# Optimization experiments

Hardware: AMD Instinct MI355X
Metric: run time of the kernel (lower is better)

## Reference

```python
import jax, jax.numpy as jnp
import numpy as np

D = 1024      # hidden_size
H = 16        # num_attention_heads
HD = D // H   # head_dim
FF = 4096     # intermediate_size
EPS = 1e-5

def layernorm(x, g, b):
    mu = jnp.mean(x, axis=-1, keepdims=True)
    var = jnp.mean(jnp.square(x - mu), axis=-1, keepdims=True)
    return (x - mu) * jax.lax.rsqrt(var + EPS) * g + b

def setup_inputs() -> dict:
    key = jax.random.key(0)
    ks = jax.random.split(key, 16)
    s = 0.02
    return {
        "x":   jax.random.normal(ks[0], (4, 1024, D), jnp.float32),
        "wq":  jax.random.normal(ks[1], (D, D), jnp.float32) * s,
        "bq":  jnp.zeros((D,), jnp.float32),
        "wk":  jax.random.normal(ks[2], (D, D), jnp.float32) * s,
        "bk":  jnp.zeros((D,), jnp.float32),
        "wv":  jax.random.normal(ks[3], (D, D), jnp.float32) * s,
        "bv":  jnp.zeros((D,), jnp.float32),
        "wo":  jax.random.normal(ks[4], (D, D), jnp.float32) * s,
        "bo":  jnp.zeros((D,), jnp.float32),
        "w1":  jax.random.normal(ks[5], (D, FF), jnp.float32) * s,
        "b1":  jnp.zeros((FF,), jnp.float32),
        "w2":  jax.random.normal(ks[6], (FF, D), jnp.float32) * s,
        "b2":  jnp.zeros((D,), jnp.float32),
        "ln1_g": jnp.ones((D,), jnp.float32),
        "ln1_b": jnp.zeros((D,), jnp.float32),
        "ln2_g": jnp.ones((D,), jnp.float32),
        "ln2_b": jnp.zeros((D,), jnp.float32),
    }

def reference(x, wq, bq, wk, bk, wv, bv, wo, bo, w1, b1, w2, b2,
              ln1_g, ln1_b, ln2_g, ln2_b):
    B, S, _ = x.shape
    # --- pre-LN multi-head attention (per-head linears fused as one GEMM) ---
    h = layernorm(x, ln1_g, ln1_b)
    q = (h @ wq + bq).reshape(B, S, H, HD).transpose(0, 2, 1, 3)  # [B,H,S,hd]
    k = (h @ wk + bk).reshape(B, S, H, HD).transpose(0, 2, 1, 3)
    v = (h @ wv + bv).reshape(B, S, H, HD).transpose(0, 2, 1, 3)
    scores = jnp.einsum('bhqd,bhkd->bhqk', q, k) / np.sqrt(HD).astype(x.dtype)
    weights = jax.nn.softmax(scores, axis=-1)  # dropout p=0 -> identity
    attn = jnp.einsum('bhqk,bhkd->bhqd', weights, v)
    attn = attn.transpose(0, 2, 1, 3).reshape(B, S, D)
    x = x + attn @ wo + bo
    # --- pre-LN feed-forward with exact GELU ---
    h2 = layernorm(x, ln2_g, ln2_b)
    ffn = jax.nn.gelu(h2 @ w1 + b1, approximate=False) @ w2 + b2
    return x + ffn
```

## Files before the change

### kernel.cpp

```cpp
#include <hip/hip_runtime.h>
#include <hip/hip_bf16.h>
#include <cstdint>

#define S_LEN  1024
#define DMODEL 1024
#define NTOK   4096
#define NHEAD  16
#define HDIM   64
#define FFDIM  4096
#define NBATCH 4
#define QSCALE 0.1803368801f

using bf16x8 = __attribute__((ext_vector_type(8))) short;
using f32x4  = __attribute__((ext_vector_type(4))) float;

__device__ __forceinline__ ushort f2bf(float f) {
  union { float f; uint32_t u; } a; a.f = f;
  uint32_t u = a.u;
  u += 0x7FFFu + ((u >> 16) & 1u);
  return (ushort)(u >> 16);
}
__device__ __forceinline__ ushort f2bf_hw(float f) {
  uint32_t r;
  asm("v_cvt_pk_bf16_f32 %0, %1, %1" : "=v"(r) : "v"(f));
  return (ushort)r;
}
__device__ __forceinline__ float bf2f(ushort u) {
  union { uint32_t u; float f; } c; c.u = ((uint32_t)u) << 16; return c.f;
}
__device__ __forceinline__ void st_out(float* C, long i, float v) { C[i] = v; }
__device__ __forceinline__ void st_out(ushort* C, long i, float v) { C[i] = f2bf(v); }

__device__ __forceinline__ void gld_lds16(const void* g, void* l) {
  __builtin_amdgcn_global_load_lds((const __attribute__((address_space(1))) void*)g,
                                   (__attribute__((address_space(3))) void*)l, 16, 0, 0);
}

__global__ __launch_bounds__(256) void ln_kernel(const float* __restrict__ x,
    const float* __restrict__ g, const float* __restrict__ b,
    ushort* __restrict__ out) {
  int row = blockIdx.x;
  int tid = threadIdx.x;
  const float4* xr = (const float4*)(x + (long)row * DMODEL);
  float4 v = xr[tid];
  float s  = v.x + v.y + v.z + v.w;
  float s2 = v.x*v.x + v.y*v.y + v.z*v.z + v.w*v.w;
  for (int off = 32; off; off >>= 1) { s += __shfl_down(s, off); s2 += __shfl_down(s2, off); }
  __shared__ float red[8];
  int wid = tid >> 6, lane = tid & 63;
  if (lane == 0) { red[wid] = s; red[wid + 4] = s2; }
  __syncthreads();
  if (tid == 0) {
    red[0] = red[0] + red[1] + red[2] + red[3];
    red[4] = red[4] + red[5] + red[6] + red[7];
  }
  __syncthreads();
  float mu  = red[0] * (1.0f / DMODEL);
  float var = red[4] * (1.0f / DMODEL) - mu * mu;
  float rs  = rsqrtf(var + 1e-5f);
  float4 gg = ((const float4*)g)[tid];
  float4 bb = ((const float4*)b)[tid];
  ushort4 o;
  o.x = f2bf((v.x - mu) * rs * gg.x + bb.x);
  o.y = f2bf((v.y - mu) * rs * gg.y + bb.y);
  o.z = f2bf((v.z - mu) * rs * gg.z + bb.z);
  o.w = f2bf((v.w - mu) * rs * gg.w + bb.w);
  ((ushort4*)(out + (long)row * DMODEL))[tid] = o;
}

__global__ __launch_bounds__(256) void concat3(const float* __restrict__ a,
    const float* __restrict__ b, const float* __restrict__ c, float* __restrict__ o) {
  int i = blockIdx.x * 256 + threadIdx.x;
  o[i] = (i < 1024) ? a[i] : ((i < 2048) ? b[i - 1024] : c[i - 2048]);
}

template <int NP>
__global__ __launch_bounds__(256) void reduce_add(
    const ushort* __restrict__ parts, const float* __restrict__ bias,
    float* __restrict__ out) {
  long i = (long)blockIdx.x * 256 + threadIdx.x;
  const long PSTRIDE = (long)NTOK * DMODEL / 4;
  float4 acc = ((const float4*)out)[i];
  float4 b = ((const float4*)bias)[i & 255];
  acc.x += b.x; acc.y += b.y; acc.z += b.z; acc.w += b.w;
#pragma unroll
  for (int z = 0; z < NP; ++z) {
    ushort4 u = ((const ushort4*)parts)[z * PSTRIDE + i];
    acc.x += bf2f(u.x); acc.y += bf2f(u.y); acc.z += bf2f(u.z); acc.w += bf2f(u.w);
  }
  ((float4*)out)[i] = acc;
}

template <int NP>
__global__ __launch_bounds__(256) void reduce_ln(
    const ushort* __restrict__ parts, const float* __restrict__ xres,
    const float* __restrict__ bias, float* __restrict__ out,
    const float* __restrict__ g, const float* __restrict__ bln,
    ushort* __restrict__ hout) {
  int row = blockIdx.x, tid = threadIdx.x;
  long i = (long)row * 256 + tid;
  const long PSTRIDE = (long)NTOK * DMODEL / 4;
  float4 v = ((const float4*)xres)[i];
  float4 b = ((const float4*)bias)[tid];
  v.x += b.x; v.y += b.y; v.z += b.z; v.w += b.w;
#pragma unroll
  for (int z = 0; z < NP; ++z) {
    ushort4 u = ((const ushort4*)parts)[z * PSTRIDE + i];
    v.x += bf2f(u.x); v.y += bf2f(u.y); v.z += bf2f(u.z); v.w += bf2f(u.w);
  }
  ((float4*)out)[i] = v;
  float s  = v.x + v.y + v.z + v.w;
  float s2 = v.x*v.x + v.y*v.y + v.z*v.z + v.w*v.w;
  for (int off = 32; off; off >>= 1) { s += __shfl_down(s, off); s2 += __shfl_down(s2, off); }
  __shared__ float red[8];
  int wid = tid >> 6, lane = tid & 63;
  if (lane == 0) { red[wid] = s; red[wid + 4] = s2; }
  __syncthreads();
  if (tid == 0) {
    red[0] = red[0] + red[1] + red[2] + red[3];
    red[4] = red[4] + red[5] + red[6] + red[7];
  }
  __syncthreads();
  float mu  = red[0] * (1.0f / DMODEL);
  float var = red[4] * (1.0f / DMODEL) - mu * mu;
  float rs  = rsqrtf(var + 1e-5f);
  float4 gg = ((const float4*)g)[tid];
  float4 bb = ((const float4*)bln)[tid];
  ushort4 o;
  o.x = f2bf((v.x - mu) * rs * gg.x + bb.x);
  o.y = f2bf((v.y - mu) * rs * gg.y + bb.y);
  o.z = f2bf((v.z - mu) * rs * gg.z + bb.z);
  o.w = f2bf((v.w - mu) * rs * gg.w + bb.w);
  ((ushort4*)hout)[i] = o;
}

template <typename TIN>
__global__ __launch_bounds__(256) void transpose_cvt(const TIN* __restrict__ in,
    ushort* __restrict__ out, int ldin, int ldout,
    long inZhi, long inZlo, long outZ) {
  int z = blockIdx.z;
  in  += (long)(z >> 4) * inZhi + (long)(z & 15) * inZlo;
  out += (long)z * outZ;
  __shared__ float tile[32][33];
  int c0 = blockIdx.x * 32, r0 = blockIdx.y * 32;
  int tx = threadIdx.x, ty = threadIdx.y;
  for (int i = ty; i < 32; i += 8)
    tile[i][tx] = bf2f(in[(long)(r0 + i) * ldin + c0 + tx]);
  __syncthreads();
  for (int i = ty; i < 32; i += 8)
    out[(long)(c0 + i) * ldout + r0 + tx] = f2bf(tile[tx][i]);
}

__global__ __launch_bounds__(256) void wt4(const float* __restrict__ wq,
    const float* __restrict__ wk, const float* __restrict__ wv,
    const float* __restrict__ wo, ushort* __restrict__ outb) {
  int z = blockIdx.z;
  const float* in = (z == 0) ? wq : (z == 1) ? wk : (z == 2) ? wv : wo;
  ushort* out = outb + (long)z * DMODEL * DMODEL;
  __shared__ float tile[32][33];
  int c0 = blockIdx.x * 32, r0 = blockIdx.y * 32;
  int tx = threadIdx.x, ty = threadIdx.y;
  for (int i = ty; i < 32; i += 8)
    tile[i][tx] = in[(long)(r0 + i) * DMODEL + c0 + tx];
  __syncthreads();
  for (int i = ty; i < 32; i += 8)
    out[(long)(c0 + i) * DMODEL + r0 + tx] = f2bf(tile[tx][i]);
}

__global__ __launch_bounds__(256) void w12t(const float* __restrict__ w1,
    const float* __restrict__ w2, ushort* __restrict__ w1T, ushort* __restrict__ w2T) {
  int z = blockIdx.z;
  __shared__ float tile[32][33];
  int tx = threadIdx.x, ty = threadIdx.y;
  if (z == 0) {
    int c0 = blockIdx.x * 32, r0 = blockIdx.y * 32;
    for (int i = ty; i < 32; i += 8)
      tile[i][tx] = w1[(long)(r0 + i) * FFDIM + c0 + tx];
    __syncthreads();
    for (int i = ty; i < 32; i += 8)
      w1T[(long)(c0 + i) * DMODEL + r0 + tx] = f2bf(tile[tx][i]);
  } else {
    int c0 = blockIdx.y * 32, r0 = blockIdx.x * 32;
    for (int i = ty; i < 32; i += 8)
      tile[i][tx] = w2[(long)(r0 + i) * DMODEL + c0 + tx];
    __syncthreads();
    for (int i = ty; i < 32; i += 8)
      w2T[(long)(c0 + i) * FFDIM + r0 + tx] = f2bf(tile[tx][i]);
  }
}

template <int ACT, bool BIAS, typename TOUT>
__global__ __launch_bounds__(256) void gemm_bt(
    const ushort* __restrict__ A, const ushort* __restrict__ BT, TOUT* __restrict__ C,
    const float* __restrict__ bias,
    int M, int K, int lda, int ldb, int ldc,
    long aZlo, long bZlo, long cZlo) {
  __shared__ __align__(16) ushort lA[2][128 * 64];
  __shared__ __align__(16) ushort lB[2][128 * 64];
  int z = blockIdx.z;
  A  += (long)z * aZlo;
  BT += (long)z * bZlo;
  C  += (long)z * cZlo;
  int gx = gridDim.x;
  int nwg = gx * gridDim.y;
  int lin = blockIdx.x + gx * blockIdx.y;
  int wg = (lin & 7) * (nwg >> 3) + (lin >> 3);
  int n0 = (wg / gx) * 128, m0 = (wg % gx) * 128;
  int tid = threadIdx.x, lane = tid & 63, wid = tid >> 6;
  int wr = wid >> 1, wc = wid & 1;
  int lrow = lane >> 3;
  int swz = ((lane & 7) ^ lrow) << 3;
  f32x4 acc[4][4];
#pragma unroll
  for (int i = 0; i < 4; i++)
#pragma unroll
    for (int j = 0; j < 4; j++) acc[i][j] = (f32x4){0.f, 0.f, 0.f, 0.f};

  long lda8 = (long)8 * lda, ldb8 = (long)8 * ldb;
  const ushort* aBase = A + (long)(n0 + wid * 32 + lrow) * lda + swz;
  const ushort* bBase = BT + (long)(m0 + wid * 32 + lrow) * ldb + swz;
  auto STAGE = [&](int kt, int buf) {
    int ko = kt << 6;
#pragma unroll
    for (int c = 0; c < 4; ++c) {
      int ch = (wid << 2) | c;
      gld_lds16(aBase + c * lda8 + ko, &lA[buf][ch << 9]);
      gld_lds16(bBase + c * ldb8 + ko, &lB[buf][ch << 9]);
    }
  };
  int kOff0 = (((lane >> 4) ^ (lane & 7)) << 3);
  int kOff1 = (((4 | (lane >> 4)) ^ (lane & 7)) << 3);

  int nK = K >> 6;
  STAGE(0, 0);
  for (int kt = 0; kt < nK; ++kt) {
    int cur = kt & 1;
    if (kt + 1 < nK) {
      STAGE(kt + 1, cur ^ 1);
      asm volatile("s_waitcnt vmcnt(8)" ::: "memory");
    } else {
      asm volatile("s_waitcnt vmcnt(0)" ::: "memory");
    }
    __builtin_amdgcn_s_barrier();
    __builtin_amdgcn_sched_barrier(0);
    const ushort* baseA = &lA[cur][((wr << 6) + (lane & 15)) * 64];
    const ushort* baseB = &lB[cur][((wc << 6) + (lane & 15)) * 64];
#pragma unroll
    for (int kk = 0; kk < 2; ++kk) {
      int kfs = kk ? kOff1 : kOff0;
      bf16x8 af[4], bfr[4];
#pragma unroll
      for (int i = 0; i < 4; i++) {
        af[i]  = *(const bf16x8*)(baseA + i * 1024 + kfs);
        bfr[i] = *(const bf16x8*)(baseB + i * 1024 + kfs);
      }
#pragma unroll
      for (int i = 0; i < 4; i++)
#pragma unroll
        for (int j = 0; j < 4; j++)
          acc[i][j] = __builtin_amdgcn_mfma_f32_16x16x32_bf16(af[i], bfr[j], acc[i][j], 0, 0, 0);
    }
    asm volatile("s_waitcnt lgkmcnt(0)" ::: "memory");
    __builtin_amdgcn_s_barrier();
    __builtin_amdgcn_sched_barrier(0);
  }
#pragma unroll
  for (int i = 0; i < 4; i++) {
    int rbase = n0 + wr * 64 + i * 16 + ((lane >> 4) << 2);
#pragma unroll
    for (int j = 0; j < 4; j++) {
      int col = m0 + wc * 64 + j * 16 + (lane & 15);
      float bv = BIAS ? bias[col] : 0.0f;
#pragma unroll
      for (int q = 0; q < 4; q++) {
        float vv = acc[i][j][q] + bv;
        if (ACT == 1) vv = 0.5f * vv * (1.0f + erff(vv * 0.70710678118f));
        if (ACT == 2 && col < DMODEL) vv *= QSCALE;
        st_out(C, (long)(rbase + q) * ldc + col, vv);
      }
    }
  }
}

template <int ACT, bool BIAS, typename TOUT>
__global__ __launch_bounds__(512, 2) void gemm256(
    const ushort* __restrict__ A, const ushort* __restrict__ BT, TOUT* __restrict__ C,
    const float* __restrict__ bias,
    int K, int lda, int ldb, int ldc, long aZlo, long bZlo, long cZlo) {
  __shared__ __align__(16) ushort lA[2][256 * 64];
  __shared__ __align__(16) ushort lB[2][256 * 64];
  int z = blockIdx.z;
  A  += (long)z * aZlo;
  BT += (long)z * bZlo;
  C  += (long)z * cZlo;
  int gx = gridDim.x;
  int nwg = gx * gridDim.y;
  int lin = blockIdx.x + gx * blockIdx.y;
  int wg = (lin & 7) * (nwg >> 3) + (lin >> 3);
  int n0 = (wg / gx) * 256, m0 = (wg % gx) * 256;
  int tid = threadIdx.x, lane = tid & 63, wid = tid >> 6;
  int wm = wid >> 2, wn = wid & 3;
  int lo = lane & 15, hi = lane >> 4;
  int l7 = lane & 7;
  int srow = tid >> 3;
  int skg  = (tid & 7) ^ (srow & 7);
  const ushort* gA = A + (long)(n0 + srow) * lda + (skg << 3);
  const ushort* gB = BT + (long)(m0 + srow) * ldb + (skg << 3);

  f32x4 acc[8][4];
#pragma unroll
  for (int i = 0; i < 8; ++i)
#pragma unroll
    for (int j = 0; j < 4; ++j) acc[i][j] = (f32x4){0.f, 0.f, 0.f, 0.f};

  auto STG = [&](int kt, int buf, int c) {
    if (c < 4)
      gld_lds16(gA + (long)(c * 64) * lda + (kt << 6), &lA[buf][c * 4096 + wid * 512]);
    else
      gld_lds16(gB + (long)((c - 4) * 64) * ldb + (kt << 6), &lB[buf][(c - 4) * 4096 + wid * 512]);
  };

  int nK = K >> 6;
  STG(0, 0, 4); STG(0, 0, 5); STG(0, 0, 6); STG(0, 0, 7);
  STG(0, 0, 0); STG(0, 0, 1); STG(0, 0, 2); STG(0, 0, 3);
  STG(1, 1, 4); STG(1, 1, 5); STG(1, 1, 6); STG(1, 1, 7);
  asm volatile("s_waitcnt vmcnt(4)" ::: "memory");
  __builtin_amdgcn_s_barrier();

  for (int t = 0; t < nK; ++t) {
    int cur = t & 1, nxt = cur ^ 1;
    ushort* plA = &lA[cur][0];
    ushort* plB = &lB[cur][0];
    bf16x8 bfr[4][2];
#pragma unroll
    for (int p = 0; p < 4; ++p) {
      if (p == 0) {
#pragma unroll
        for (int j = 0; j < 4; ++j)
#pragma unroll
          for (int kk = 0; kk < 2; ++kk)
            bfr[j][kk] = *(const bf16x8*)&plB[(wn * 64 + j * 16 + lo) * 64 +
                                             ((((kk << 2) | hi) ^ l7) << 3)];
      }
      bf16x8 afr[2][2];
#pragma unroll
      for (int ii = 0; ii < 2; ++ii)
#pragma unroll
        for (int kk = 0; kk < 2; ++kk)
          afr[ii][kk] = *(const bf16x8*)&plA[(wm * 128 + (p * 2 + ii) * 16 + lo) * 64 +
                                             ((((kk << 2) | hi) ^ l7) << 3)];
      if (p == 0 && t + 1 < nK) { STG(t + 1, nxt, 0); STG(t + 1, nxt, 1); }
      if (p == 1 && t + 1 < nK) { STG(t + 1, nxt, 2); STG(t + 1, nxt, 3); }
      if (p == 2 && t + 2 < nK) { STG(t + 2, cur, 4); STG(t + 2, cur, 5); }
      if (p == 3 && t + 2 < nK) { STG(t + 2, cur, 6); STG(t + 2, cur, 7); }
      __builtin_amdgcn_s_barrier();
      asm volatile("s_waitcnt lgkmcnt(0)" ::: "memory");
      __builtin_amdgcn_sched_barrier(0);
      __builtin_amdgcn_s_setprio(1);
#pragma unroll
      for (int ii = 0; ii < 2; ++ii)
#pragma unroll
        for (int j = 0; j < 4; ++j)
#pragma unroll
          for (int kk = 0; kk < 2; ++kk)
            acc[p * 2 + ii][j] = __builtin_amdgcn_mfma_f32_16x16x32_bf16(
                afr[ii][kk], bfr[j][kk], acc[p * 2 + ii][j], 0, 0, 0);
      __builtin_amdgcn_s_setprio(0);
      __builtin_amdgcn_sched_barrier(0);
      if (p == 3 && t + 1 < nK) {
        if (t + 2 < nK) asm volatile("s_waitcnt vmcnt(4)" ::: "memory");
        else            asm volatile("s_waitcnt vmcnt(0)" ::: "memory");
      }
      __builtin_amdgcn_s_barrier();
    }
  }

#pragma unroll
  for (int i = 0; i < 8; ++i) {
    int rbase = n0 + wm * 128 + i * 16 + hi * 4;
#pragma unroll
    for (int j = 0; j < 4; ++j) {
      int colg = m0 + wn * 64 + j * 16 + lo;
      float bv = BIAS ? bias[colg] : 0.0f;
#pragma unroll
      for (int q = 0; q < 4; ++q) {
        float vv = acc[i][j][q] + bv;
        if (ACT == 1) vv = 0.5f * vv * (1.0f + erff(vv * 0.70710678118f));
        if (ACT == 2 && colg < DMODEL) vv *= QSCALE;
        long idx = (long)(rbase + q) * ldc + colg;
        st_out(C, idx, vv);
      }
    }
  }
}

#define QBLK 128
#define KBLK 128
__global__ __launch_bounds__(512) void flash_attn(
    const ushort* __restrict__ qkv, const ushort* __restrict__ vt,
    ushort* __restrict__ attn) {
  __shared__ __align__(16) ushort lK[2][KBLK * 64];
  __shared__ __align__(16) ushort lV[2][64 * KBLK];
  __shared__ __align__(16) ushort lP[8 * 16 * KBLK];

  int qt = blockIdx.x, bh = blockIdx.z;
  int b = bh >> 4, hh = bh & 15;
  int tid = threadIdx.x, lane = tid & 63, wid = tid >> 6;
  int lo = lane & 15, hi = lane >> 4;
  int lrow = lane >> 3;
  int swz8 = ((lane & 7) ^ lrow) << 3;

  const ushort* Qg = qkv + (long)(b * 1024 + qt * QBLK) * 3072 + hh * 64;
  const ushort* Kg = qkv + (long)(b * 1024) * 3072 + 1024 + hh * 64;
  const ushort* Vg = vt + (long)bh * 64 * 1024;
  ushort* lPw = lP + wid * (16 * KBLK);

  bf16x8 kOnes;
#pragma unroll
  for (int i = 0; i < 8; ++i) kOnes[i] = (short)0x3F80;

  auto STAGE = [&](int t, int buf) {
#pragma unroll
    for (int c = 0; c < 2; ++c) {
      int ch = (wid << 1) | c;
      int rb = (ch << 3) + lrow;
      gld_lds16(Kg + (long)(t * KBLK + rb) * 3072 + swz8, &lK[buf][ch << 9]);
    }
#pragma unroll
    for (int c = 0; c < 2; ++c) {
      int ch = (wid << 1) | c;
      int hd = (ch << 2) + hi;
      gld_lds16(Vg + (long)hd * 1024 + t * KBLK + ((lo ^ (hd & 7)) << 3), &lV[buf][ch << 9]);
    }
  };

#pragma unroll
  for (int c = 0; c < 2; ++c) {
    int ch = (wid << 1) | c;
    int rb = (ch << 3) + lrow;
    gld_lds16(Qg + (long)rb * 3072 + swz8, &lP[ch << 9]);
  }
  STAGE(0, 0);
  asm volatile("s_waitcnt vmcnt(4)" ::: "memory");
  __builtin_amdgcn_sched_barrier(0);
  bf16x8 a_q[2];
#pragma unroll
  for (int kk = 0; kk < 2; ++kk)
    a_q[kk] = *(const bf16x8*)&lP[(wid * 16 + lo) * 64 + (((kk * 4 + hi) ^ (lo & 7)) << 3)];
  asm volatile("s_waitcnt lgkmcnt(0)" ::: "memory");
  __builtin_amdgcn_sched_barrier(0);
  __builtin_amdgcn_s_barrier();

  float m_run[4];
#pragma unroll
  for (int q = 0; q < 4; ++q) m_run[q] = -1e30f;
  f32x4 acc_o[4];
#pragma unroll
  for (int j = 0; j < 4; ++j) acc_o[j] = (f32x4){0.f, 0.f, 0.f, 0.f};
  f32x4 acc_l = (f32x4){0.f, 0.f, 0.f, 0.f};

  for (int t = 0; t < 8; ++t) {
    int cur = t & 1;
    if (t + 1 < 8) {
      STAGE(t + 1, cur ^ 1);
      asm volatile("s_waitcnt vmcnt(4)" ::: "memory");
    } else {
      asm volatile("s_waitcnt vmcnt(0)" ::: "memory");
    }
    __builtin_amdgcn_s_barrier();
    __builtin_amdgcn_sched_barrier(0);

    f32x4 s[8];
#pragma unroll
    for (int j = 0; j < 8; ++j) s[j] = (f32x4){0.f, 0.f, 0.f, 0.f};
    __builtin_amdgcn_s_setprio(1);
#pragma unroll
    for (int kk = 0; kk < 2; ++kk) {
      int slot = ((kk * 4 + hi) ^ (lo & 7)) << 3;
#pragma unroll
      for (int j = 0; j < 8; ++j) {
        bf16x8 bk = *(const bf16x8*)&lK[cur][(j * 16 + lo) * 64 + slot];
        s[j] = __builtin_amdgcn_mfma_f32_16x16x32_bf16(a_q[kk], bk, s[j], 0, 0, 0);
      }
    }
    __builtin_amdgcn_s_setprio(0);

    float alpha[4];
#pragma unroll
    for (int q = 0; q < 4; ++q) {
      float m = fmaxf(fmaxf(fmaxf(s[0][q], s[1][q]), fmaxf(s[2][q], s[3][q])),
                      fmaxf(fmaxf(s[4][q], s[5][q]), fmaxf(s[6][q], s[7][q])));
#pragma unroll
      for (int off = 1; off < 16; off <<= 1) m = fmaxf(m, __shfl_xor(m, off));
      float mnew = fmaxf(m_run[q], m);
      alpha[q] = __builtin_amdgcn_exp2f(m_run[q] - mnew);
      m_run[q] = mnew;
    }
#pragma unroll
    for (int j = 0; j < 8; ++j)
#pragma unroll
      for (int q = 0; q < 4; ++q) {
        float e = __builtin_amdgcn_exp2f(s[j][q] - m_run[q]);
        int row = hi * 4 + q;
        int col = j * 16 + lo;
        lPw[row * KBLK + (col ^ ((row & 7) << 3))] = f2bf_hw(e);
      }

#pragma unroll
    for (int q = 0; q < 4; ++q) acc_l[q] *= alpha[q];
#pragma unroll
    for (int j = 0; j < 4; ++j)
#pragma unroll
      for (int q = 0; q < 4; ++q) acc_o[j][q] *= alpha[q];
    __builtin_amdgcn_s_setprio(1);
#pragma unroll
    for (int ks = 0; ks < 4; ++ks) {
      int slot = ((ks * 4 + hi) ^ (lo & 7)) << 3;
      bf16x8 ap = *(const bf16x8*)&lPw[lo * KBLK + slot];
      acc_l = __builtin_amdgcn_mfma_f32_16x16x32_bf16(ap, kOnes, acc_l, 0, 0, 0);
#pragma unroll
      for (int j = 0; j < 4; ++j) {
        bf16x8 bv = *(const bf16x8*)&lV[cur][(j * 16 + lo) * KBLK + slot];
        acc_o[j] = __builtin_amdgcn_mfma_f32_16x16x32_bf16(ap, bv, acc_o[j], 0, 0, 0);
      }
    }
    __builtin_amdgcn_s_setprio(0);
    asm volatile("s_waitcnt lgkmcnt(0)" ::: "memory");
    __builtin_amdgcn_s_barrier();
    __builtin_amdgcn_sched_barrier(0);
  }

#pragma unroll
  for (int q = 0; q < 4; ++q) {
    float linv = 1.0f / acc_l[q];
    int qrow = qt * QBLK + wid * 16 + hi * 4 + q;
#pragma unroll
    for (int j = 0; j < 4; ++j)
      attn[(long)(b * 1024 + qrow) * 1024 + hh * 64 + j * 16 + lo] = f2bf(acc_o[j][q] * linv);
  }
}

extern "C" void kernel_launch(void* const* d_in, const int* in_sizes, int n_in,
                              void* d_out, int out_size, void* d_ws, size_t ws_size,
                              hipStream_t stream) {
  const float* x    = (const float*)d_in[0];
  const float* wq   = (const float*)d_in[1];
  const float* bq   = (const float*)d_in[2];
  const float* wk   = (const float*)d_in[3];
  const float* bk   = (const float*)d_in[4];
  const float* wv   = (const float*)d_in[5];
  const float* bv   = (const float*)d_in[6];
  const float* wo   = (const float*)d_in[7];
  const float* bo   = (const float*)d_in[8];
  const float* w1   = (const float*)d_in[9];
  const float* b1   = (const float*)d_in[10];
  const float* w2   = (const float*)d_in[11];
  const float* b2   = (const float*)d_in[12];
  const float* ln1g = (const float*)d_in[13];
  const float* ln1b = (const float*)d_in[14];
  const float* ln2g = (const float*)d_in[15];
  const float* ln2b = (const float*)d_in[16];
  float* out = (float*)d_out;

  char* ws = (char*)d_ws;
  size_t off = 0;
  auto alloc = [&](size_t bytes) { void* p = ws + off; off += (bytes + 255) & ~(size_t)255; return p; };
  ushort* h     = (ushort*)alloc((size_t)NTOK * DMODEL * 2);
  ushort* wqkvT = (ushort*)alloc((size_t)3 * DMODEL * DMODEL * 2);
  ushort* woT   = (ushort*)alloc((size_t)DMODEL * DMODEL * 2);
  float*  bqkv  = (float*)alloc((size_t)3 * DMODEL * 4);
  ushort* qkv   = (ushort*)alloc((size_t)NTOK * 3 * DMODEL * 2);
  ushort* vt    = (ushort*)alloc((size_t)64 * HDIM * S_LEN * 2);
  ushort* attn  = (ushort*)alloc((size_t)NTOK * DMODEL * 2);
  ushort* w1T   = (ushort*)alloc((size_t)DMODEL * FFDIM * 2);
  ushort* w2T   = (ushort*)alloc((size_t)FFDIM * DMODEL * 2);
  ushort* gact  = (ushort*)alloc((size_t)NTOK * FFDIM * 2);
  ushort* woPart  = qkv;
  ushort* ffnPart = qkv;

  dim3 tb32(32, 8);
  hipLaunchKernelGGL(wt4, dim3(DMODEL/32, DMODEL/32, 4), tb32, 0, stream,
                     wq, wk, wv, wo, wqkvT);
  hipLaunchKernelGGL(w12t, dim3(FFDIM/32, DMODEL/32, 2), tb32, 0, stream,
                     w1, w2, w1T, w2T);
  hipLaunchKernelGGL(concat3, dim3(12), dim3(256), 0, stream, bq, bk, bv, bqkv);

  hipLaunchKernelGGL(ln_kernel, dim3(NTOK), dim3(256), 0, stream, x, ln1g, ln1b, h);

  hipLaunchKernelGGL((gemm256<2, true, ushort>), dim3(12, 16, 1), dim3(512), 0, stream,
                     h, wqkvT, qkv, bqkv, DMODEL, DMODEL, DMODEL, 3 * DMODEL, 0L, 0L, 0L);

  hipLaunchKernelGGL((transpose_cvt<ushort>), dim3(HDIM/32, S_LEN/32, 64), tb32, 0, stream,
                     qkv + 2 * DMODEL, vt, 3 * DMODEL, S_LEN,
                     (long)S_LEN * 3 * DMODEL, 64L, (long)HDIM * S_LEN);

  hipLaunchKernelGGL(flash_attn, dim3(8, 1, 64), dim3(512), 0, stream, qkv, vt, attn);

  hipLaunchKernelGGL((gemm_bt<0, false, ushort>), dim3(8, 32, 2), dim3(256), 0, stream,
                     attn, woT, woPart, (const float*)nullptr,
                     DMODEL, 512, DMODEL, DMODEL, DMODEL,
                     512L, 512L, (long)NTOK * DMODEL);
  hipLaunchKernelGGL((reduce_ln<2>), dim3(4096), dim3(256), 0, stream,
                     woPart, x, bo, out, ln2g, ln2b, h);
  hipLaunchKernelGGL((gemm256<1, true, ushort>), dim3(16, 16, 1), dim3(512), 0, stream,
                     h, w1T, gact, b1, DMODEL, DMODEL, DMODEL, FFDIM, 0L, 0L, 0L);
  hipLaunchKernelGGL((gemm256<0, false, ushort>), dim3(4, 16, 4), dim3(512), 0, stream,
                     gact, w2T, ffnPart, (const float*)nullptr,
                     1024, FFDIM, FFDIM, DMODEL, 1024L, 1024L, (long)NTOK * DMODEL);
  hipLaunchKernelGGL((reduce_add<4>), dim3(4096), dim3(256), 0, stream,
                     ffnPart, b2, out);
  (void)in_sizes; (void)n_in; (void)out_size; (void)ws_size;
}
```

Before: 244.5 us.

## Single-buffer gemm256 LDS and raise launch bounds to four blocks per CU

Drops the double-buffered LDS pipeline in the 256x256 GEMM in favour of a simple load, sync, compute, sync loop with one shared buffer each for A and B. It also raises the launch-bounds occupancy hint from 2 to 4 blocks, aiming to hide memory latency through more resident workgroups rather than software prefetch. The cost is losing the overlap of global loads with MFMA work. The 4-block hint also forces a very small per-wave register budget for a kernel holding 128 accumulator values, which risks spills, while the LDS use likely still limits residency to fewer blocks than hinted.

New measurement: 906.0 us. +270.5%, slower.

```diff
diff --git a/kernel.cpp b/kernel.cpp
--- a/kernel.cpp
+++ b/kernel.cpp
@@ -283,12 +283,12 @@
 }
 
 template <int ACT, bool BIAS, typename TOUT>
-__global__ __launch_bounds__(512, 2) void gemm256(
+__global__ __launch_bounds__(512, 4) void gemm256(
     const ushort* __restrict__ A, const ushort* __restrict__ BT, TOUT* __restrict__ C,
     const float* __restrict__ bias,
     int K, int lda, int ldb, int ldc, long aZlo, long bZlo, long cZlo) {
-  __shared__ __align__(16) ushort lA[2][256 * 64];
-  __shared__ __align__(16) ushort lB[2][256 * 64];
+  __shared__ __align__(16) ushort lA[256 * 64];
+  __shared__ __align__(16) ushort lB[256 * 64];
   int z = blockIdx.z;
   A  += (long)z * aZlo;
   BT += (long)z * bZlo;
@@ -306,6 +306,7 @@
   int skg  = (tid & 7) ^ (srow & 7);
   const ushort* gA = A + (long)(n0 + srow) * lda + (skg << 3);
   const ushort* gB = BT + (long)(m0 + srow) * ldb + (skg << 3);
+  long lda64 = (long)64 * lda, ldb64 = (long)64 * ldb;
 
   f32x4 acc[8][4];
 #pragma unroll
@@ -313,50 +314,34 @@
 #pragma unroll
     for (int j = 0; j < 4; ++j) acc[i][j] = (f32x4){0.f, 0.f, 0.f, 0.f};
 
-  auto STG = [&](int kt, int buf, int c) {
-    if (c < 4)
-      gld_lds16(gA + (long)(c * 64) * lda + (kt << 6), &lA[buf][c * 4096 + wid * 512]);
-    else
-      gld_lds16(gB + (long)((c - 4) * 64) * ldb + (kt << 6), &lB[buf][(c - 4) * 4096 + wid * 512]);
-  };
+  int kOff0 = ((hi ^ l7) << 3);
+  int kOff1 = (((4 | hi) ^ l7) << 3);
 
   int nK = K >> 6;
-  STG(0, 0, 4); STG(0, 0, 5); STG(0, 0, 6); STG(0, 0, 7);
-  STG(0, 0, 0); STG(0, 0, 1); STG(0, 0, 2); STG(0, 0, 3);
-  STG(1, 1, 4); STG(1, 1, 5); STG(1, 1, 6); STG(1, 1, 7);
-  asm volatile("s_waitcnt vmcnt(4)" ::: "memory");
-  __builtin_amdgcn_s_barrier();
-
   for (int t = 0; t < nK; ++t) {
-    int cur = t & 1, nxt = cur ^ 1;
-    ushort* plA = &lA[cur][0];
-    ushort* plB = &lB[cur][0];
+    int ko = t << 6;
+#pragma unroll
+    for (int c = 0; c < 4; ++c) {
+      gld_lds16(gA + c * lda64 + ko, &lA[c * 4096 + wid * 512]);
+      gld_lds16(gB + c * ldb64 + ko, &lB[c * 4096 + wid * 512]);
+    }
+    __syncthreads();
+    const ushort* baseA = &lA[(wm * 128 + lo) * 64];
+    const ushort* baseB = &lB[(wn * 64 + lo) * 64];
     bf16x8 bfr[4][2];
 #pragma unroll
+    for (int j = 0; j < 4; ++j) {
+      bfr[j][0] = *(const bf16x8*)(baseB + j * 1024 + kOff0);
+      bfr[j][1] = *(const bf16x8*)(baseB + j * 1024 + kOff1);
+    }
+#pragma unroll
     for (int p = 0; p < 4; ++p) {
-      if (p == 0) {
-#pragma unroll
-        for (int j = 0; j < 4; ++j)
-#pragma unroll
-          for (int kk = 0; kk < 2; ++kk)
-            bfr[j][kk] = *(const bf16x8*)&plB[(wn * 64 + j * 16 + lo) * 64 +
-                                             ((((kk << 2) | hi) ^ l7) << 3)];
-      }
       bf16x8 afr[2][2];
 #pragma unroll
-      for (int ii = 0; ii < 2; ++ii)
-#pragma unroll
-        for (int kk = 0; kk < 2; ++kk)
-          afr[ii][kk] = *(const bf16x8*)&plA[(wm * 128 + (p * 2 + ii) * 16 + lo) * 64 +
-                                             ((((kk << 2) | hi) ^ l7) << 3)];
-      if (p == 0 && t + 1 < nK) { STG(t + 1, nxt, 0); STG(t + 1, nxt, 1); }
-      if (p == 1 && t + 1 < nK) { STG(t + 1, nxt, 2); STG(t + 1, nxt, 3); }
-      if (p == 2 && t + 2 < nK) { STG(t + 2, cur, 4); STG(t + 2, cur, 5); }
-      if (p == 3 && t + 2 < nK) { STG(t + 2, cur, 6); STG(t + 2, cur, 7); }
-      __builtin_amdgcn_s_barrier();
-      asm volatile("s_waitcnt lgkmcnt(0)" ::: "memory");
-      __builtin_amdgcn_sched_barrier(0);
-      __builtin_amdgcn_s_setprio(1);
+      for (int ii = 0; ii < 2; ++ii) {
+        afr[ii][0] = *(const bf16x8*)(baseA + (p * 2 + ii) * 1024 + kOff0);
+        afr[ii][1] = *(const bf16x8*)(baseA + (p * 2 + ii) * 1024 + kOff1);
+      }
 #pragma unroll
       for (int ii = 0; ii < 2; ++ii)
 #pragma unroll
@@ -365,14 +350,8 @@
           for (int kk = 0; kk < 2; ++kk)
             acc[p * 2 + ii][j] = __builtin_amdgcn_mfma_f32_16x16x32_bf16(
                 afr[ii][kk], bfr[j][kk], acc[p * 2 + ii][j], 0, 0, 0);
-      __builtin_amdgcn_s_setprio(0);
-      __builtin_amdgcn_sched_barrier(0);
-      if (p == 3 && t + 1 < nK) {
-        if (t + 2 < nK) asm volatile("s_waitcnt vmcnt(4)" ::: "memory");
-        else            asm volatile("s_waitcnt vmcnt(0)" ::: "memory");
-      }
-      __builtin_amdgcn_s_barrier();
-    }
+    }
+    __syncthreads();
   }
 
 #pragma unroll
```
